# Kernel tuning notes

Hardware: AMD Instinct MI355X
Metric: run time of the kernel (lower is better)

The kernel has to match this reference:

```python
import jax, jax.numpy as jnp
import numpy as np
from jax import lax

EPS = 1e-6

def rms_norm(x, w):
    return x * lax.rsqrt(jnp.mean(x * x, axis=-1, keepdims=True) + EPS) * w

def rec_layer(x, conv_w, conv_b, Wr_w, Wr_b, Wi_w, Wi_b, log_a, out_w, norm_w):
    # x: [B, L, d]; depthwise causal conv, kernel size 4
    B, L, d = x.shape
    xc = lax.conv_general_dilated(
        x.transpose(0, 2, 1), conv_w, window_strides=(1,), padding=[(3, 0)],
        dimension_numbers=("NCH", "OIH", "NCH"), feature_group_count=d)
    x_conv = xc.transpose(0, 2, 1) + conv_b  # [B, L, d]
    r_t = jax.nn.sigmoid(x_conv @ Wr_w.T + Wr_b)
    i_t = jax.nn.sigmoid(x_conv @ Wi_w.T + Wi_b)
    a_base = jax.nn.sigmoid(log_a)  # [d]
    a_t = jnp.power(a_base, 8.0 * r_t)  # [B, L, d]
    u_t = i_t * x_conv

    def step(h, au):
        a, u = au
        h = a * h + jnp.sqrt(jnp.clip(1.0 - a * a, 0.0, None)) * u
        return h, h

    _, hs = lax.scan(step, jnp.zeros((B, d), x.dtype),
                     (a_t.transpose(1, 0, 2), u_t.transpose(1, 0, 2)))
    out = hs.transpose(1, 0, 2)  # [B, L, d]
    return rms_norm(out @ out_w.T, norm_w)

def setup_inputs() -> dict:
    B, L, M, d, do = 8, 2048, 256, 1024, 256
    key = jax.random.key(0)
    ks = jax.random.split(key, 24)
    inp = {
        "concept_out": jax.random.normal(ks[0], (B, M, d), jnp.float32),
        "encoder_out": jax.random.normal(ks[1], (B, L, d), jnp.float32),
        "boundary_probs": jax.random.uniform(ks[2], (B, L), jnp.float32),
        "boundary_idx": jnp.sort(jax.random.randint(ks[3], (B, M), 0, L, jnp.int32), axis=1),
        "gate_w": jax.random.normal(ks[4], (d, d), jnp.float32) * 0.02,
        "gate_b": jnp.zeros((d,), jnp.float32),
        "down_w": jax.random.normal(ks[5], (do, d), jnp.float32) * 0.02,
        "up_w": jax.random.normal(ks[6], (d, do), jnp.float32) * 0.02,
        "norm_out_w": jnp.ones((d,), jnp.float32),
        "rec_conv_w": jax.random.normal(ks[7], (3, do, 1, 4), jnp.float32) * 0.02,
        "rec_conv_b": jnp.zeros((3, do), jnp.float32),
        "rec_Wr_w": jax.random.normal(ks[8], (3, do, do), jnp.float32) * 0.02,
        "rec_Wr_b": jnp.zeros((3, do), jnp.float32),
        "rec_Wi_w": jax.random.normal(ks[9], (3, do, do), jnp.float32) * 0.02,
        "rec_Wi_b": jnp.zeros((3, do), jnp.float32),
        "rec_log_a": jnp.full((3, do), 7.5, jnp.float32),
        "rec_out_w": jax.random.normal(ks[10], (3, do, do), jnp.float32) * 0.02,
        "rec_norm_w": jnp.ones((3, do), jnp.float32),
    }
    return inp

def reference(concept_out, encoder_out, boundary_probs, boundary_idx,
              gate_w, gate_b, down_w, up_w, norm_out_w,
              rec_conv_w, rec_conv_b, rec_Wr_w, rec_Wr_b,
              rec_Wi_w, rec_Wi_b, rec_log_a, rec_out_w, rec_norm_w):
    B, L, d = encoder_out.shape
    M = concept_out.shape[1]
    # 1. EMA smoothing over boundaries
    p_at_bounds = jnp.take_along_axis(boundary_probs, boundary_idx, axis=1)  # [B, M]

    def ema_step(h, pc):
        p_i, c_i = pc  # [B], [B, d]
        h = p_i[:, None] * c_i + (1.0 - p_i[:, None]) * h
        return h, h

    _, sm = lax.scan(ema_step, jnp.zeros((B, d), concept_out.dtype),
                     (p_at_bounds.T, concept_out.transpose(1, 0, 2)))
    smoothed = sm.transpose(1, 0, 2)  # [B, M, d]
    # 2. Plug-back via searchsorted (== torch.bucketize right=True)
    arange_L = jnp.arange(L)
    counts = jax.vmap(lambda bi: jnp.searchsorted(bi, arange_L, side="right"))(boundary_idx)
    bucket = jnp.clip(counts - 1, 0, None)  # [B, L]
    plugback = jnp.take_along_axis(smoothed, bucket[..., None], axis=1)  # [B, L, d]
    # 3. Gated residual
    gate = jax.nn.sigmoid(encoder_out @ gate_w.T + gate_b)
    h = (1.0 - boundary_probs[..., None]) * gate * encoder_out + plugback
    # 4. Decoder recurrence
    h = h @ down_w.T
    for k in range(3):
        h = rec_layer(h, rec_conv_w[k], rec_conv_b[k], rec_Wr_w[k], rec_Wr_b[k],
                      rec_Wi_w[k], rec_Wi_b[k], rec_log_a[k], rec_out_w[k], rec_norm_w[k])
    h = h @ up_w.T
    return rms_norm(h, norm_out_w)
```

## Files before the change

### kernel.cpp

```cpp
#include <hip/hip_runtime.h>
#include <hip/hip_bf16.h>
#include <stdint.h>

typedef __attribute__((ext_vector_type(8))) short short8;
typedef __attribute__((ext_vector_type(4))) float f32x4;
typedef __hip_bfloat16 bf16;

#define NB   8
#define LSEQ 2048
#define NM   256
#define DMODEL 1024
#define DO   256
#define BLR  16384
#define NCH  32
#define CLK  64

__device__ __forceinline__ float sigm(float x) { return 1.f / (1.f + __expf(-x)); }

__device__ __forceinline__ void gl_lds16(const void* g, void* l) {
  __builtin_amdgcn_global_load_lds((const __attribute__((address_space(1))) void*)g,
                                   (__attribute__((address_space(3))) void*)l, 16, 0, 0);
}

__device__ __forceinline__ unsigned short bf16bits(float v) {
  bf16 b = __float2bfloat16(v);
  return *(unsigned short*)&b;
}
__device__ __forceinline__ float bits2f(unsigned short u) {
  bf16 b = *(bf16*)&u;
  return __bfloat162float(b);
}


__global__ __launch_bounds__(256) void prep_kernel(
    const float* __restrict__ gate_w, const float* __restrict__ down_w,
    const float* __restrict__ up_w, const float* __restrict__ wr_w,
    const float* __restrict__ wi_w, const float* __restrict__ ow_w,
    const float* __restrict__ log_a,
    bf16* __restrict__ gate_wb, bf16* __restrict__ down_wb, bf16* __restrict__ up_wb,
    bf16* __restrict__ wrb, bf16* __restrict__ wib, bf16* __restrict__ owb,
    float* __restrict__ e8) {
  int i = blockIdx.x * 256 + threadIdx.x;
  if (i < 1048576) { gate_wb[i] = __float2bfloat16(gate_w[i]); return; }
  i -= 1048576;
  if (i < 262144) { down_wb[i] = __float2bfloat16(down_w[i]); return; }
  i -= 262144;
  if (i < 262144) { up_wb[i] = __float2bfloat16(up_w[i]); return; }
  i -= 262144;
  if (i < 196608) { wrb[i] = __float2bfloat16(wr_w[i]); return; }
  i -= 196608;
  if (i < 196608) { wib[i] = __float2bfloat16(wi_w[i]); return; }
  i -= 196608;
  if (i < 196608) { owb[i] = __float2bfloat16(ow_w[i]); return; }
  i -= 196608;
  if (i < 768) {
    float ab = 1.f / (1.f + expf(-log_a[i]));
    e8[i] = 8.f * log2f(ab);
  }
}

__global__ __launch_bounds__(256) void cvt4_kernel(const float4* __restrict__ in,
                                                   ushort4* __restrict__ out, int n4) {
  int i = blockIdx.x * 256 + threadIdx.x;
  if (i < n4) {
    float4 v = in[i];
    ushort4 o;
    o.x = bf16bits(v.x); o.y = bf16bits(v.y); o.z = bf16bits(v.z); o.w = bf16bits(v.w);
    out[i] = o;
  }
}


__global__ __launch_bounds__(256) void ema_kernel(const float* __restrict__ cpt,
                                                  const float* __restrict__ bprobs,
                                                  const int* __restrict__ bidx,
                                                  float* __restrict__ smoothed) {
  int b = blockIdx.x >> 2;
  int c = ((blockIdx.x & 3) << 8) + threadIdx.x;
  __shared__ float p[NM];
  p[threadIdx.x] = bprobs[b * LSEQ + bidx[b * NM + threadIdx.x]];
  __syncthreads();
  const float* cp = cpt + (size_t)b * NM * DMODEL + c;
  float* sp = smoothed + (size_t)b * NM * DMODEL + c;
  float h = 0.f;
  for (int m = 0; m < NM; ++m) {
    float pm = p[m];
    h = pm * cp[(size_t)m * DMODEL] + (1.f - pm) * h;
    sp[(size_t)m * DMODEL] = h;
  }
}

__global__ __launch_bounds__(256) void bucket_kernel(const int* __restrict__ bidx,
                                                     int* __restrict__ bucket) {
  int i = blockIdx.x * 256 + threadIdx.x;
  int b = i >> 11, l = i & 2047;
  const int* bi = bidx + b * NM;
  int lo = 0, hi = NM;
  while (lo < hi) {
    int mid = (lo + hi) >> 1;
    if (bi[mid] <= l) lo = mid + 1; else hi = mid;
  }
  int v = lo - 1;
  bucket[i] = v < 0 ? 0 : v;
}


__global__ __launch_bounds__(256) void conv_kernel(const bf16* __restrict__ x,
                                                   const float* __restrict__ cw,
                                                   const float* __restrict__ cb,
                                                   bf16* __restrict__ xcb) {
  int i = blockIdx.x * 256 + threadIdx.x;
  int c = i & 255;
  int bl = i >> 8;
  int l = bl & 2047;
  float4 w4 = ((const float4*)cw)[c];
  const float* wf = (const float*)&w4;
  float s = cb[c];
#pragma unroll
  for (int kk = 0; kk < 4; ++kk) {
    int ll = l - 3 + kk;
    if (ll >= 0) s += wf[kk] * __bfloat162float(x[i + (kk - 3) * 256]);
  }
  xcb[i] = __float2bfloat16(s);
}


__global__ __launch_bounds__(256) void scan_p1(const unsigned int* __restrict__ ds,
                                               float2* __restrict__ AS) {
  int b = blockIdx.x >> 5, ch = blockIdx.x & 31, c = threadIdx.x;
  size_t base = ((size_t)b * LSEQ + ch * CLK) * DO + c;
  float A = 1.f, S = 0.f;
  for (int t = 0; t < CLK; ++t) {
    unsigned int u = ds[base + (size_t)t * DO];
    float d = bits2f((unsigned short)(u & 0xffff));
    float s = bits2f((unsigned short)(u >> 16));
    float a = 1.f - d;
    A *= a;
    S = __builtin_fmaf(a, S, s);
  }
  AS[blockIdx.x * DO + c] = make_float2(A, S);
}

__global__ __launch_bounds__(256) void scan_p2(const unsigned int* __restrict__ ds,
                                               const float2* __restrict__ AS,
                                               bf16* __restrict__ hs) {
  int b = blockIdx.x >> 5, ch = blockIdx.x & 31, c = threadIdx.x;
  float h = 0.f;
  for (int j = 0; j < ch; ++j) {
    float2 as = AS[(b * NCH + j) * DO + c];
    h = __builtin_fmaf(as.x, h, as.y);
  }
  size_t base = ((size_t)b * LSEQ + ch * CLK) * DO + c;
  for (int t = 0; t < CLK; ++t) {
    unsigned int u = ds[base + (size_t)t * DO];
    float d = bits2f((unsigned short)(u & 0xffff));
    float s = bits2f((unsigned short)(u >> 16));
    h = __builtin_fmaf(-d, h, h) + s;
    hs[base + (size_t)t * DO] = __float2bfloat16(h);
  }
}


__global__ __launch_bounds__(256) void rmsnorm1024_kernel(const bf16* __restrict__ in,
                                                          const float* __restrict__ w,
                                                          float* __restrict__ out) {
  int row = blockIdx.x, t = threadIdx.x;
  ushort4 raw = ((const ushort4*)(in + (size_t)row * 1024))[t];
  float v0 = bits2f(raw.x), v1 = bits2f(raw.y), v2 = bits2f(raw.z), v3 = bits2f(raw.w);
  float ss = v0 * v0 + v1 * v1 + v2 * v2 + v3 * v3;
#pragma unroll
  for (int ofs = 32; ofs > 0; ofs >>= 1) ss += __shfl_down(ss, ofs, 64);
  __shared__ float wsum[4];
  if ((t & 63) == 0) wsum[t >> 6] = ss;
  __syncthreads();
  float tot = wsum[0] + wsum[1] + wsum[2] + wsum[3];
  float sc = rsqrtf(tot * (1.f / 1024.f) + 1e-6f);
  float4 wv = ((const float4*)w)[t];
  float4 o;
  o.x = v0 * sc * wv.x; o.y = v1 * sc * wv.y;
  o.z = v2 * sc * wv.z; o.w = v3 * sc * wv.w;
  ((float4*)(out + (size_t)row * 1024))[t] = o;
}


struct EpA {
  bf16* outb;
  const float* bias;
  const bf16* encb;
  const float* p;
  const int* bucket;
  const float* smoothed;
};

template <int EP>
__global__ __launch_bounds__(256) void gemm_bt(const bf16* __restrict__ A,
                                               const bf16* __restrict__ W,
                                               int N, int K, EpA ep) {
  __shared__ __align__(16) bf16 As[128 * 64];
  __shared__ __align__(16) bf16 Bs[128 * 64];
  const int t = threadIdx.x;
  const int lane = t & 63;
  const int wv = t >> 6;
  const int wm = wv >> 1, wn = wv & 1;
  const int quad = lane >> 4, l16 = lane & 15;
  const int bm = blockIdx.x << 7, bn = blockIdx.y << 7;

  f32x4 acc[4][4] = {};

  for (int k0 = 0; k0 < K; k0 += 64) {
    __syncthreads();
#pragma unroll
    for (int i = 0; i < 4; ++i) {
      int slot = i * 256 + t;
      int m = slot >> 3;
      int lk8 = (slot & 7) ^ (m & 7);
      gl_lds16(A + (size_t)(bm + m) * K + k0 + lk8 * 8, As + slot * 8);
      gl_lds16(W + (size_t)(bn + m) * K + k0 + lk8 * 8, Bs + slot * 8);
    }
    __syncthreads();
#pragma unroll
    for (int ks = 0; ks < 2; ++ks) {
      short8 af[4], bfr[4];
#pragma unroll
      for (int i = 0; i < 4; ++i) {
        int m = wm * 64 + i * 16 + l16;
        int pa = (ks * 4 + quad) ^ (m & 7);
        af[i] = *(const short8*)(As + m * 64 + pa * 8);
        int n = wn * 64 + i * 16 + l16;
        int pb = (ks * 4 + quad) ^ (n & 7);
        bfr[i] = *(const short8*)(Bs + n * 64 + pb * 8);
      }
#pragma unroll
      for (int i = 0; i < 4; ++i)
#pragma unroll
        for (int j = 0; j < 4; ++j)
          acc[i][j] = __builtin_amdgcn_mfma_f32_16x16x32_bf16(af[i], bfr[j], acc[i][j], 0, 0, 0);
    }
  }

#pragma unroll
  for (int i = 0; i < 4; ++i) {
#pragma unroll
    for (int j = 0; j < 4; ++j) {
#pragma unroll
      for (int r = 0; r < 4; ++r) {
        int m = bm + wm * 64 + i * 16 + quad * 4 + r;
        int n = bn + wn * 64 + j * 16 + l16;
        size_t idx = (size_t)m * N + n;
        float v = acc[i][j][r];
        if (EP == 1) {
          float g = sigm(v + ep.bias[n]);
          float pm = ep.p[m];
          int bb = m >> 11;
          float sm = ep.smoothed[((size_t)(bb * NM + ep.bucket[m])) * DMODEL + n];
          float e = __bfloat162float(ep.encb[idx]);
          ep.outb[idx] = __float2bfloat16((1.f - pm) * g * e + sm);
        } else {
          ep.outb[idx] = __float2bfloat16(v);
        }
      }
    }
  }
}


__global__ __launch_bounds__(256) void gemm_ri(const bf16* __restrict__ A,
                                               const bf16* __restrict__ Wr,
                                               const bf16* __restrict__ Wi,
                                               const float* __restrict__ rbias,
                                               const float* __restrict__ ibias,
                                               const float* __restrict__ e8,
                                               unsigned int* __restrict__ ds_out) {
  __shared__ __align__(16) bf16 As[128 * 64];
  __shared__ __align__(16) bf16 Br[128 * 64];
  __shared__ __align__(16) bf16 Bi[128 * 64];
  const int t = threadIdx.x;
  const int lane = t & 63;
  const int wv = t >> 6;
  const int wm = wv >> 1, wn = wv & 1;
  const int quad = lane >> 4, l16 = lane & 15;
  const int bm = blockIdx.x << 7, bn = blockIdx.y << 7;

  f32x4 ar[4][4] = {};
  f32x4 ai[4][4] = {};

  for (int k0 = 0; k0 < DO; k0 += 64) {
    __syncthreads();
#pragma unroll
    for (int i = 0; i < 4; ++i) {
      int slot = i * 256 + t;
      int m = slot >> 3;
      int lk8 = (slot & 7) ^ (m & 7);
      gl_lds16(A + (size_t)(bm + m) * DO + k0 + lk8 * 8, As + slot * 8);
      gl_lds16(Wr + (size_t)(bn + m) * DO + k0 + lk8 * 8, Br + slot * 8);
      gl_lds16(Wi + (size_t)(bn + m) * DO + k0 + lk8 * 8, Bi + slot * 8);
    }
    __syncthreads();
#pragma unroll
    for (int ks = 0; ks < 2; ++ks) {
      short8 af[4], br[4], bi[4];
#pragma unroll
      for (int i = 0; i < 4; ++i) {
        int m = wm * 64 + i * 16 + l16;
        int pa = (ks * 4 + quad) ^ (m & 7);
        af[i] = *(const short8*)(As + m * 64 + pa * 8);
        int n = wn * 64 + i * 16 + l16;
        int pb = (ks * 4 + quad) ^ (n & 7);
        br[i] = *(const short8*)(Br + n * 64 + pb * 8);
        bi[i] = *(const short8*)(Bi + n * 64 + pb * 8);
      }
#pragma unroll
      for (int i = 0; i < 4; ++i)
#pragma unroll
        for (int j = 0; j < 4; ++j) {
          ar[i][j] = __builtin_amdgcn_mfma_f32_16x16x32_bf16(af[i], br[j], ar[i][j], 0, 0, 0);
          ai[i][j] = __builtin_amdgcn_mfma_f32_16x16x32_bf16(af[i], bi[j], ai[i][j], 0, 0, 0);
        }
    }
  }

#pragma unroll
  for (int i = 0; i < 4; ++i) {
#pragma unroll
    for (int j = 0; j < 4; ++j) {
#pragma unroll
      for (int r = 0; r < 4; ++r) {
        int m = bm + wm * 64 + i * 16 + quad * 4 + r;
        int n = bn + wn * 64 + j * 16 + l16;
        size_t idx = (size_t)m * DO + n;
        float rv = sigm(ar[i][j][r] + rbias[n]);
        float a = exp2f(rv * e8[n]);
        float d = 1.f - a;
        float iv = sigm(ai[i][j][r] + ibias[n]);
        float xc = __bfloat162float(A[idx]);
        float s = sqrtf(fmaxf(1.f - a * a, 0.f)) * iv * xc;
        ds_out[idx] = (unsigned int)bf16bits(d) | ((unsigned int)bf16bits(s) << 16);
      }
    }
  }
}


__global__ __launch_bounds__(256) void gemm_on(const bf16* __restrict__ A,
                                               const bf16* __restrict__ W,
                                               const float* __restrict__ rnw,
                                               bf16* __restrict__ xb) {
  __shared__ __align__(16) bf16 As[64 * 64];
  __shared__ __align__(16) bf16 Bs[256 * 64];
  __shared__ float red[4][64];
  const int t = threadIdx.x;
  const int lane = t & 63;
  const int wn = t >> 6;
  const int quad = lane >> 4, l16 = lane & 15;
  const int bm = blockIdx.x << 6;

  f32x4 acc[4][4] = {};

  for (int k0 = 0; k0 < DO; k0 += 64) {
    __syncthreads();
#pragma unroll
    for (int i = 0; i < 2; ++i) {
      int slot = i * 256 + t;
      int m = slot >> 3;
      int lk8 = (slot & 7) ^ (m & 7);
      gl_lds16(A + (size_t)(bm + m) * DO + k0 + lk8 * 8, As + slot * 8);
    }
#pragma unroll
    for (int i = 0; i < 8; ++i) {
      int slot = i * 256 + t;
      int n = slot >> 3;
      int lk8 = (slot & 7) ^ (n & 7);
      gl_lds16(W + (size_t)n * DO + k0 + lk8 * 8, Bs + slot * 8);
    }
    __syncthreads();
#pragma unroll
    for (int ks = 0; ks < 2; ++ks) {
      short8 af[4], bfr[4];
#pragma unroll
      for (int i = 0; i < 4; ++i) {
        int m = i * 16 + l16;
        int pa = (ks * 4 + quad) ^ (m & 7);
        af[i] = *(const short8*)(As + m * 64 + pa * 8);
        int n = wn * 64 + i * 16 + l16;
        int pb = (ks * 4 + quad) ^ (n & 7);
        bfr[i] = *(const short8*)(Bs + n * 64 + pb * 8);
      }
#pragma unroll
      for (int i = 0; i < 4; ++i)
#pragma unroll
        for (int j = 0; j < 4; ++j)
          acc[i][j] = __builtin_amdgcn_mfma_f32_16x16x32_bf16(af[i], bfr[j], acc[i][j], 0, 0, 0);
    }
  }

  float part[4][4];
#pragma unroll
  for (int i = 0; i < 4; ++i)
#pragma unroll
    for (int r = 0; r < 4; ++r) {
      float s = 0.f;
#pragma unroll
      for (int j = 0; j < 4; ++j) s += acc[i][j][r] * acc[i][j][r];
      part[i][r] = s;
    }
#pragma unroll
  for (int mask = 1; mask <= 8; mask <<= 1)
#pragma unroll
    for (int i = 0; i < 4; ++i)
#pragma unroll
      for (int r = 0; r < 4; ++r) part[i][r] += __shfl_xor(part[i][r], mask, 64);
  if (l16 == 0) {
#pragma unroll
    for (int i = 0; i < 4; ++i)
#pragma unroll
      for (int r = 0; r < 4; ++r) red[wn][i * 16 + quad * 4 + r] = part[i][r];
  }
  __syncthreads();
#pragma unroll
  for (int i = 0; i < 4; ++i) {
#pragma unroll
    for (int r = 0; r < 4; ++r) {
      int ml = i * 16 + quad * 4 + r;
      float tot = red[0][ml] + red[1][ml] + red[2][ml] + red[3][ml];
      float sc = rsqrtf(tot * (1.f / 256.f) + 1e-6f);
#pragma unroll
      for (int j = 0; j < 4; ++j) {
        int n = wn * 64 + j * 16 + l16;
        xb[(size_t)(bm + ml) * DO + n] = __float2bfloat16(acc[i][j][r] * sc * rnw[n]);
      }
    }
  }
}


extern "C" void kernel_launch(void* const* d_in, const int* in_sizes, int n_in,
                              void* d_out, int out_size, void* d_ws, size_t ws_size,
                              hipStream_t stream) {
  const float* concept_out = (const float*)d_in[0];
  const float* encoder_out = (const float*)d_in[1];
  const float* bprobs      = (const float*)d_in[2];
  const int*   bidx        = (const int*)d_in[3];
  const float* gate_w      = (const float*)d_in[4];
  const float* gate_b      = (const float*)d_in[5];
  const float* down_w      = (const float*)d_in[6];
  const float* up_w        = (const float*)d_in[7];
  const float* norm_out_w  = (const float*)d_in[8];
  const float* rc_w        = (const float*)d_in[9];
  const float* rc_b        = (const float*)d_in[10];
  const float* wr_w        = (const float*)d_in[11];
  const float* wr_b        = (const float*)d_in[12];
  const float* wi_w        = (const float*)d_in[13];
  const float* wi_b        = (const float*)d_in[14];
  const float* log_a       = (const float*)d_in[15];
  const float* ow_w        = (const float*)d_in[16];
  const float* rn_w        = (const float*)d_in[17];
  float* out = (float*)d_out;
  (void)in_sizes; (void)n_in; (void)out_size; (void)ws_size;

  char* base = (char*)d_ws;
  size_t off = 0;
  auto alloc = [&](size_t bytes) -> char* {
    char* p = base + off;
    off += (bytes + 255) & ~(size_t)255;
    return p;
  };
  float* smoothed = (float*)alloc((size_t)NB * NM * DMODEL * 4);
  int*   bucket   = (int*)alloc((size_t)BLR * 4);
  bf16*  gate_wb  = (bf16*)alloc((size_t)DMODEL * DMODEL * 2);
  bf16*  down_wb  = (bf16*)alloc((size_t)DO * DMODEL * 2);
  bf16*  up_wb    = (bf16*)alloc((size_t)DMODEL * DO * 2);
  bf16*  wrb      = (bf16*)alloc((size_t)3 * DO * DO * 2);
  bf16*  wib      = (bf16*)alloc((size_t)3 * DO * DO * 2);
  bf16*  owb      = (bf16*)alloc((size_t)3 * DO * DO * 2);
  float* e8       = (float*)alloc(3 * DO * 4);
  float2* ASsum   = (float2*)alloc((size_t)NB * NCH * DO * 8);
  bf16*  xb       = (bf16*)alloc((size_t)BLR * DO * 2);

  const size_t SZ_ENC   = (size_t)BLR * DMODEL * 2;
  const size_t SZ_XCONV = (size_t)BLR * DO * 2;
  const size_t SZ_DS    = (size_t)BLR * DO * 4;
  char* RA = alloc(2 * SZ_ENC);
  bf16*  encb = (bf16*)RA;
  bf16*  h0b  = (bf16*)(RA + SZ_ENC);
  bf16*         xconvb = (bf16*)RA;
  unsigned int* dsbuf  = (unsigned int*)(RA + SZ_XCONV);
  bf16*         hsb    = (bf16*)(RA + SZ_XCONV + SZ_DS);
  bf16*  tmp2b  = (bf16*)RA;

  cvt4_kernel<<<(BLR * DMODEL / 4 + 255) / 256, 256, 0, stream>>>(
      (const float4*)encoder_out, (ushort4*)encb, BLR * DMODEL / 4);
  prep_kernel<<<(2163456 + 255) / 256, 256, 0, stream>>>(
      gate_w, down_w, up_w, wr_w, wi_w, ow_w, log_a,
      gate_wb, down_wb, up_wb, wrb, wib, owb, e8);
  ema_kernel<<<NB * 4, 256, 0, stream>>>(concept_out, bprobs, bidx, smoothed);
  bucket_kernel<<<BLR / 256, 256, 0, stream>>>(bidx, bucket);

  EpA ep;
  ep = EpA{};
  ep.outb = h0b; ep.bias = gate_b; ep.encb = encb; ep.p = bprobs;
  ep.bucket = bucket; ep.smoothed = smoothed;
  gemm_bt<1><<<dim3(BLR / 128, DMODEL / 128), 256, 0, stream>>>(encb, gate_wb, DMODEL, DMODEL, ep);
  ep = EpA{}; ep.outb = xb;
  gemm_bt<5><<<dim3(BLR / 128, DO / 128), 256, 0, stream>>>(h0b, down_wb, DO, DMODEL, ep);

  for (int k = 0; k < 3; ++k) {
    conv_kernel<<<BLR, 256, 0, stream>>>(xb, rc_w + k * DO * 4, rc_b + k * DO, xconvb);
    gemm_ri<<<dim3(BLR / 128, DO / 128), 256, 0, stream>>>(
        xconvb, wrb + k * DO * DO, wib + k * DO * DO,
        wr_b + k * DO, wi_b + k * DO, e8 + k * DO, dsbuf);
    scan_p1<<<NB * NCH, 256, 0, stream>>>(dsbuf, ASsum);
    scan_p2<<<NB * NCH, 256, 0, stream>>>(dsbuf, ASsum, hsb);
    gemm_on<<<BLR / 64, 256, 0, stream>>>(hsb, owb + k * DO * DO, rn_w + k * DO, xb);
  }

  ep = EpA{}; ep.outb = tmp2b;
  gemm_bt<5><<<dim3(BLR / 128, DMODEL / 128), 256, 0, stream>>>(xb, up_wb, DMODEL, DO, ep);
  rmsnorm1024_kernel<<<BLR, 256, 0, stream>>>(tmp2b, norm_out_w, out);
}
```

Measured before the change: 533.3 us.

## Add 256x256 double-buffered pipelined GEMM for gate and up projections

Adds a new 512-thread GEMM kernel with 256x256 output tiles. It double-buffers LDS through direct global-to-LDS loads, interleaves staging of the next K tile with MFMA phases, and raises MFMA priority with setprio. The gate GEMM (16384x1024x1024) and the up projection (K=256) now use it instead of the 128x128 kernel. The aim is more data reuse per tile and latency hiding for the largest GEMMs, at the cost of register pressure, fewer blocks (256 total) for occupancy, and a complex hand-scheduled pipeline.

```diff
diff --git a/kernel.cpp b/kernel.cpp
--- a/kernel.cpp
+++ b/kernel.cpp
@@ -192,6 +192,7 @@
   const float* smoothed;
 };
 
+
 template <int EP>
 __global__ __launch_bounds__(256) void gemm_bt(const bf16* __restrict__ A,
                                                const bf16* __restrict__ W,
@@ -245,6 +246,153 @@
 #pragma unroll
       for (int r = 0; r < 4; ++r) {
         int m = bm + wm * 64 + i * 16 + quad * 4 + r;
+        int n = bn + wn * 64 + j * 16 + l16;
+        size_t idx = (size_t)m * N + n;
+        float v = acc[i][j][r];
+        if (EP == 1) {
+          float g = sigm(v + ep.bias[n]);
+          float pm = ep.p[m];
+          int bb = m >> 11;
+          float sm = ep.smoothed[((size_t)(bb * NM + ep.bucket[m])) * DMODEL + n];
+          float e = __bfloat162float(ep.encb[idx]);
+          ep.outb[idx] = __float2bfloat16((1.f - pm) * g * e + sm);
+        } else {
+          ep.outb[idx] = __float2bfloat16(v);
+        }
+      }
+    }
+  }
+}
+
+
+template <int EP>
+__global__ __launch_bounds__(512, 2) void gemm256(const bf16* __restrict__ Ag,
+                                                  const bf16* __restrict__ W,
+                                                  int N, int K, EpA ep) {
+  __shared__ __align__(16) bf16 lds[2][4][128 * 64];
+  const int t = threadIdx.x;
+  const int lane = t & 63;
+  const int wv = t >> 6;
+  const int wm = wv >> 2, wn = wv & 3;
+  const int quad = lane >> 4, l16 = lane & 15;
+  const int bm = blockIdx.x << 8, bn = blockIdx.y << 8;
+  const int KT = K >> 6;
+  const int KM = KT - 1;
+
+  const int rr = t >> 3;
+  const int cc = (t & 7) ^ (rr & 7);
+
+  f32x4 acc[8][4] = {};
+  short8 af[4][2], bfr[2][2];
+
+#define STAGE_A(BUF, H, KTI)                                                      \
+  {                                                                               \
+    int kk = ((KTI) & KM) << 6;                                                   \
+    const bf16* s0 = Ag + (size_t)(bm + (H) * 64 + rr) * K + kk + cc * 8;         \
+    gl_lds16(s0, &lds[BUF][H][t * 8]);                                            \
+    const bf16* s1 = Ag + (size_t)(bm + (H) * 64 + rr + 128) * K + kk + cc * 8;   \
+    gl_lds16(s1, &lds[BUF][H][(512 + t) * 8]);                                    \
+  }
+#define STAGE_B(BUF, H, KTI)                                                      \
+  {                                                                               \
+    int kk = ((KTI) & KM) << 6;                                                   \
+    int n0 = (H) * 32 + (rr & 31) + ((rr >> 5) << 6);                             \
+    const bf16* s0 = W + (size_t)(bn + n0) * K + kk + cc * 8;                     \
+    gl_lds16(s0, &lds[BUF][2 + (H)][t * 8]);                                      \
+    const bf16* s1 = W + (size_t)(bn + n0 + 128) * K + kk + cc * 8;               \
+    gl_lds16(s1, &lds[BUF][2 + (H)][(512 + t) * 8]);                              \
+  }
+#define LD_A(BUF, MG)                                                             \
+  _Pragma("unroll") for (int ii = 0; ii < 4; ++ii) {                              \
+    int r = wm * 64 + ii * 16 + l16;                                              \
+    _Pragma("unroll") for (int ks = 0; ks < 2; ++ks) {                            \
+      int ch = (ks * 4 + quad) ^ (r & 7);                                         \
+      af[ii][ks] = *(const short8*)&lds[BUF][MG][(r * 8 + ch) * 8];               \
+    }                                                                             \
+  }
+#define LD_B(BUF, NG)                                                             \
+  _Pragma("unroll") for (int jj = 0; jj < 2; ++jj) {                              \
+    int r = wn * 32 + jj * 16 + l16;                                              \
+    _Pragma("unroll") for (int ks = 0; ks < 2; ++ks) {                            \
+      int ch = (ks * 4 + quad) ^ (r & 7);                                         \
+      bfr[jj][ks] = *(const short8*)&lds[BUF][2 + (NG)][(r * 8 + ch) * 8];        \
+    }                                                                             \
+  }
+#define MMA(MG, NG)                                                               \
+  _Pragma("unroll") for (int ks = 0; ks < 2; ++ks)                                \
+  _Pragma("unroll") for (int ii = 0; ii < 4; ++ii)                                \
+  _Pragma("unroll") for (int jj = 0; jj < 2; ++jj)                                \
+    acc[(MG) * 4 + ii][(NG) * 2 + jj] = __builtin_amdgcn_mfma_f32_16x16x32_bf16(  \
+        af[ii][ks], bfr[jj][ks], acc[(MG) * 4 + ii][(NG) * 2 + jj], 0, 0, 0);
+#define BARR __builtin_amdgcn_s_barrier()
+#define WAIT_LGKM asm volatile("s_waitcnt lgkmcnt(0)" ::: "memory")
+#define WAIT_VM4 asm volatile("s_waitcnt vmcnt(4)" ::: "memory")
+#define PH(MG, NG)                   \
+  BARR; WAIT_LGKM;                   \
+  __builtin_amdgcn_s_setprio(1);     \
+  MMA(MG, NG);                       \
+  __builtin_amdgcn_s_setprio(0);     \
+  BARR;
+#define PH_V(MG, NG)                 \
+  BARR; WAIT_LGKM;                   \
+  __builtin_amdgcn_s_setprio(1);     \
+  MMA(MG, NG);                       \
+  __builtin_amdgcn_s_setprio(0);     \
+  WAIT_VM4;                          \
+  BARR;
+
+  STAGE_A(0, 0, 0) STAGE_A(0, 1, 0) STAGE_B(0, 0, 0) STAGE_B(0, 1, 0)
+  STAGE_A(1, 0, 1) STAGE_B(1, 1, 1)
+  WAIT_VM4;
+  BARR;
+
+#pragma unroll 1
+  for (int it = 0; it < (KT >> 1); ++it) {
+    const int kt = it * 2;
+    LD_A(0, 0) LD_B(0, 0)
+    STAGE_A(1, 1, kt + 1)
+    PH(0, 0)
+    LD_B(0, 1)
+    STAGE_B(1, 0, kt + 1)
+    PH(0, 1)
+    LD_A(0, 1)
+    STAGE_A(0, 0, kt + 2)
+    PH(1, 1)
+    LD_B(0, 0)
+    STAGE_B(0, 1, kt + 2)
+    PH_V(1, 0)
+    LD_A(1, 0) LD_B(1, 0)
+    STAGE_A(0, 1, kt + 2)
+    PH(0, 0)
+    LD_B(1, 1)
+    STAGE_B(0, 0, kt + 2)
+    PH(0, 1)
+    LD_A(1, 1)
+    STAGE_A(1, 0, kt + 3)
+    PH(1, 1)
+    LD_B(1, 0)
+    STAGE_B(1, 1, kt + 3)
+    PH_V(1, 0)
+  }
+
+#undef STAGE_A
+#undef STAGE_B
+#undef LD_A
+#undef LD_B
+#undef MMA
+#undef BARR
+#undef WAIT_LGKM
+#undef WAIT_VM4
+#undef PH
+#undef PH_V
+
+#pragma unroll
+  for (int i = 0; i < 8; ++i) {
+#pragma unroll
+    for (int j = 0; j < 4; ++j) {
+#pragma unroll
+      for (int r = 0; r < 4; ++r) {
+        int m = bm + wm * 128 + i * 16 + quad * 4 + r;
         int n = bn + wn * 64 + j * 16 + l16;
         size_t idx = (size_t)m * N + n;
         float v = acc[i][j][r];
@@ -499,7 +647,7 @@
   ep = EpA{};
   ep.outb = h0b; ep.bias = gate_b; ep.encb = encb; ep.p = bprobs;
   ep.bucket = bucket; ep.smoothed = smoothed;
-  gemm_bt<1><<<dim3(BLR / 128, DMODEL / 128), 256, 0, stream>>>(encb, gate_wb, DMODEL, DMODEL, ep);
+  gemm256<1><<<dim3(BLR / 256, DMODEL / 256), 512, 0, stream>>>(encb, gate_wb, DMODEL, DMODEL, ep);
   ep = EpA{}; ep.outb = xb;
   gemm_bt<5><<<dim3(BLR / 128, DO / 128), 256, 0, stream>>>(h0b, down_wb, DO, DMODEL, ep);
 
@@ -514,6 +662,6 @@
   }
 
   ep = EpA{}; ep.outb = tmp2b;
-  gemm_bt<5><<<dim3(BLR / 128, DMODEL / 128), 256, 0, stream>>>(xb, up_wb, DMODEL, DO, ep);
+  gemm256<5><<<dim3(BLR / 256, DMODEL / 256), 512, 0, stream>>>(xb, up_wb, DMODEL, DO, ep);
   rmsnorm1024_kernel<<<BLR, 256, 0, stream>>>(tmp2b, norm_out_w, out);
 }
```

Result: no change. 534.4 us (+0.2%).
